# Performance work log

Measured on AMD Instinct MI355X. Metric: run time of the kernel, lower is better.

The kernel has to match this reference:

```python
import jax, jax.numpy as jnp
import numpy as np

# Module config (matches init_kwargs)
T = 4096          # max_seq_length == runtime seq len
L = 1024          # local_size
BQ = 16           # block_q (q bucket size in flash loop)
BK = 128          # block_k (k bucket size in flash loop)
C = 128           # query chunk size used for the banded jax formulation (multiple of BQ, == BK)
NC = T // C       # number of query chunks
W = L + C         # key window width per query chunk: [chunk_start - L, chunk_start + C)
HEAD_DIM = 64
NUM_HEAD = 16
SCALE = 1.0 / float(np.sqrt(HEAD_DIM))


def _build_mask():
    # Reproduces the flash path's sparsity: a (q,k) pair is kept iff
    #   j <= i  (element-level causal) AND
    #   k_block_start(j) >= q_block_start(i) - local_size  (block skip rule)
    # where q_block_start = (i//BQ)*BQ, k_block_start = (j//BK)*BK.
    i_loc = np.arange(C)                      # query offset inside chunk
    j_rel = np.arange(W) - L                  # key offset relative to chunk start
    causal = j_rel[None, :] <= i_loc[:, None]
    kb = (j_rel // BK) * BK                   # floor-div works for negatives
    qb = (i_loc // BQ) * BQ
    local_ok = kb[None, :] >= qb[:, None] - L
    static = causal & local_ok                # [C, W], chunk-independent
    starts = np.arange(NC) * C
    valid = (starts[:, None] + j_rel[None, :]) >= 0   # mask out left padding
    return jnp.asarray(static[None, :, :] & valid[:, None, :])  # [NC, C, W]

MASK = _build_mask()


def setup_inputs() -> dict:
    key = jax.random.key(0)
    k1, k2, k3 = jax.random.split(key, 3)
    B = 2
    E = NUM_HEAD * HEAD_DIM
    q = jax.random.normal(k1, (T, B, E), jnp.float32)
    k = jax.random.normal(k2, (T, B, E), jnp.float32)
    v = jax.random.normal(k3, (T, B, E), jnp.float32)
    padding_mask = jnp.zeros((B, T), bool)     # unused by module's forward
    attention_mask = jnp.zeros((B, T), bool)   # unused by module's forward
    return {"q": q, "k": k, "v": v, "padding_mask": padding_mask, "attention_mask": attention_mask}


def _attend(qh, kh, vh):
    # qh/kh/vh: [BH, T, D]; banded local+causal attention
    BH, _, D = qh.shape
    qr = (qh * SCALE).reshape(BH, NC, C, D)
    kp = jnp.pad(kh, ((0, 0), (L, 0), (0, 0)))
    vp = jnp.pad(vh, ((0, 0), (L, 0), (0, 0)))
    # window gather: chunk c covers padded indices [c*C, c*C + W)
    idx = jnp.arange(NC)[:, None] * C + jnp.arange(W)[None, :]   # [NC, W]
    kw = kp[:, idx]   # [BH, NC, W, D]
    vw = vp[:, idx]   # [BH, NC, W, D]
    s = jnp.einsum('bcid,bcjd->bcij', qr, kw)      # [BH, NC, C, W]
    s = jnp.where(MASK, s, -jnp.inf)
    p = jax.nn.softmax(s, axis=-1)                 # every row has a valid (diagonal) entry
    o = jnp.einsum('bcij,bcjd->bcid', p, vw)
    return o.reshape(BH, T, D)


def reference(q, k, v, padding_mask, attention_mask):
    Tq, B, E = q.shape
    # (T, B, H*D) -> (B*H, T, D), matching view(T, B*H, D).transpose(0,1)
    qh = q.reshape(Tq, B * NUM_HEAD, HEAD_DIM).transpose(1, 0, 2)
    kh = k.reshape(Tq, B * NUM_HEAD, HEAD_DIM).transpose(1, 0, 2)
    vh = v.reshape(Tq, B * NUM_HEAD, HEAD_DIM).transpose(1, 0, 2)
    o = _attend(qh, kh, vh)                        # [B*H, T, D]
    # out.transpose(0,1).view(T, B, H*D)
    return o.transpose(1, 0, 2).reshape(Tq, B, E)
```

## Files before the change

### kernel.cpp

```cpp
#include <hip/hip_runtime.h>
#include <hip/hip_bf16.h>

typedef float f32x16 __attribute__((ext_vector_type(16)));
typedef short bf16x8 __attribute__((ext_vector_type(8)));

#define SCALE2 0.1803368801111242f

#define EXP2(x) __builtin_amdgcn_exp2f(x)

static __device__ __forceinline__ unsigned int pk2(float a, float b) {
  unsigned short lo = __builtin_bit_cast(unsigned short, __float2bfloat16(a));
  unsigned short hi = __builtin_bit_cast(unsigned short, __float2bfloat16(b));
  return (unsigned int)lo | ((unsigned int)hi << 16);
}

#define GLDS16(g, l) __builtin_amdgcn_global_load_lds(                      \
    (const __attribute__((address_space(1))) unsigned int*)(g),             \
    (__attribute__((address_space(3))) unsigned int*)(l), 16, 0, 0)

extern "C" __global__ __launch_bounds__(256)
void prep_qk(const float* __restrict__ q, const float* __restrict__ k,
             char* __restrict__ qs, char* __restrict__ ks)
{
  int idx = blockIdx.x * 256 + threadIdx.x;
  const bool isK = idx >= (1 << 20);
  idx &= (1 << 20) - 1;
  const int fb  = idx * 8;
  const int t   = fb >> 11;
  const int rem = fb & 2047;
  const int bh  = rem >> 6;
  const int d0  = rem & 63;
  const float* sp = (isK ? k : q) + fb;
  const float4 f0 = *(const float4*)sp;
  const float4 f1 = *(const float4*)(sp + 4);
  uint4 u;
  if (isK) {
    u.x = pk2(f0.x, f0.y); u.y = pk2(f0.z, f0.w);
    u.z = pk2(f1.x, f1.y); u.w = pk2(f1.z, f1.w);
    const size_t ob = (size_t)bh * 524288 + (size_t)t * 128 + ((d0 * 2) ^ ((t & 7) << 4));
    *(uint4*)(ks + ob) = u;
  } else {
    u.x = pk2(f0.x * SCALE2, f0.y * SCALE2); u.y = pk2(f0.z * SCALE2, f0.w * SCALE2);
    u.z = pk2(f1.x * SCALE2, f1.y * SCALE2); u.w = pk2(f1.z * SCALE2, f1.w * SCALE2);
    const size_t ob = (size_t)bh * 524288 + (size_t)t * 128 + d0 * 2;
    *(uint4*)(qs + ob) = u;
  }
}

extern "C" __global__ __launch_bounds__(256)
void prep_v(const float* __restrict__ v, char* __restrict__ vts)
{
  __shared__ float Lt[64 * 65];
  const int bh   = blockIdx.x >> 6;
  const int tile = blockIdx.x & 63;
  const int t0   = tile * 64;
  const int b = bh >> 4, h = bh & 15;
  const float* vp = v + (size_t)t0 * 2048 + b * 1024 + h * 64;
  const int tid = threadIdx.x;
  const int dd = tid & 63, tl = tid >> 6;
  #pragma unroll
  for (int p2 = 0; p2 < 16; ++p2) {
    const int t_loc = p2 * 4 + tl;
    Lt[dd * 65 + t_loc] = vp[(size_t)t_loc * 2048 + dd];
  }
  __syncthreads();
  const int d = tid >> 2, tg = tid & 3;
  float a[16];
  #pragma unroll
  for (int j = 0; j < 16; ++j) a[j] = Lt[d * 65 + tg * 16 + j];
  uint4 u0, u1;
  u0.x = pk2(a[0], a[1]);  u0.y = pk2(a[2], a[3]);
  u0.z = pk2(a[4], a[5]);  u0.w = pk2(a[6], a[7]);
  u1.x = pk2(a[8], a[9]);  u1.y = pk2(a[10], a[11]);
  u1.z = pk2(a[12], a[13]); u1.w = pk2(a[14], a[15]);
  const size_t ob = (size_t)bh * 524288 + (size_t)d * 8192;
  const int off0 = t0 * 2 + tg * 32;
  const int swz = (d & 7) << 4;
  *(uint4*)(vts + ob + ((off0) ^ swz))      = u0;
  *(uint4*)(vts + ob + ((off0 + 16) ^ swz)) = u1;
}

extern "C" __global__ __launch_bounds__(256, 4)
void sparse_attn7(const char* __restrict__ qs, const char* __restrict__ ks,
                  const char* __restrict__ vts, float* __restrict__ og)
{
  __shared__ __align__(16) char lds[32768];

  const int w    = blockIdx.x;
  const int work = (w & 7) * 128 + (w >> 3);
  const int c    = work & 31;
  const int bh   = work >> 5;

  const int tid = threadIdx.x;
  const int wv  = tid >> 6;
  const int ln  = tid & 63;
  const int l31 = ln & 31;
  const int hi  = ln >> 5;

  const int ql = wv * 32 + l31;
  const int qt = c * 128 + ql;
  const size_t hb = (size_t)bh * 524288;

  bf16x8 qf[4];
  {
    const char* qp = qs + hb + (size_t)qt * 128 + hi * 16;
    #pragma unroll
    for (int kd = 0; kd < 4; ++kd)
      qf[kd] = *(const bf16x8*)(qp + kd * 32);
  }

  f32x16 ot[2];
  #pragma unroll
  for (int i = 0; i < 2; ++i)
    #pragma unroll
    for (int r = 0; r < 16; ++r) ot[i][r] = 0.f;

  float lsum = 0.f;

  const int n0 = (c >= 8) ? 0 : (16 - 2 * c);

  const char* kga = ks  + hb + (size_t)((2 * c - 16 + n0) * 64) * 128
                    + (wv * 2) * 1024 + ln * 16;
  const char* vga = vts + hb + (size_t)((wv * 2) * 8 + (ln >> 3)) * 8192
                    + (size_t)((2 * c - 16 + n0) * 64) * 2 + (ln & 7) * 16;

  auto STAGE = [&](int p) {
    char* kl = lds + p * 16384 + wv * 2048;
    char* vl = lds + p * 16384 + 8192 + wv * 2048;
    GLDS16(kga,            kl);
    GLDS16(kga + 1024,     kl + 1024);
    GLDS16(vga,            vl);
    GLDS16(vga + 8 * 8192, vl + 1024);
  };

  STAGE(0);
  kga += 8192; vga += 128;
  __syncthreads();

  int p = 0;
  for (int n = n0; n <= 17; ++n) {
    if (n < 17) {
      STAGE(p ^ 1);
      kga += 8192; vga += 128;
    }

    const bool skip = ((n <= 1) && (wv > 0)) || ((n == 17) && (wv < 2));
    if (!skip) {
      const char* Kl = lds + p * 16384;
      const char* Vt = lds + p * 16384 + 8192;

      f32x16 st[2];
      #pragma unroll
      for (int mt = 0; mt < 2; ++mt)
        #pragma unroll
        for (int r = 0; r < 16; ++r) st[mt][r] = 0.f;

      __builtin_amdgcn_s_setprio(1);
      #pragma unroll
      for (int kd = 0; kd < 4; ++kd) {
        #pragma unroll
        for (int mt = 0; mt < 2; ++mt) {
          const int key  = mt * 32 + l31;
          const int boff = (key * 128 + kd * 32 + hi * 16) ^ ((key & 7) << 4);
          const bf16x8 kf = *(const bf16x8*)(Kl + boff);
          st[mt] = __builtin_amdgcn_mfma_f32_32x32x16_bf16(kf, qf[kd], st[mt], 0, 0, 0);
        }
      }
      __builtin_amdgcn_s_setprio(0);

      if (n >= 16 && wv * 32 < (n - 16) * 64 + 64) {
        const int base = (n - 16) * 64;
        #pragma unroll
        for (int mt = 0; mt < 2; ++mt)
          #pragma unroll
          for (int r = 0; r < 16; ++r) {
            const int kl2 = base + mt * 32 + (r & 3) + 8 * (r >> 2) + 4 * hi;
            if (kl2 > ql) st[mt][r] = -1e30f;
          }
      }

      const bool dead = (n <= 1) && (l31 >= 16);
      if (!dead) {
        #pragma unroll
        for (int mt = 0; mt < 2; ++mt)
          #pragma unroll
          for (int r = 0; r < 16; ++r)
            st[mt][r] = EXP2(st[mt][r]);
      } else {
        #pragma unroll
        for (int mt = 0; mt < 2; ++mt)
          #pragma unroll
          for (int r = 0; r < 16; ++r) st[mt][r] = 0.f;
      }

      #pragma unroll
      for (int mt = 0; mt < 2; ++mt) {
        #pragma unroll
        for (int s = 0; s < 2; ++s) {
          const unsigned int X0 = pk2(st[mt][s * 8 + 0], st[mt][s * 8 + 1]);
          const unsigned int X1 = pk2(st[mt][s * 8 + 2], st[mt][s * 8 + 3]);
          const unsigned int Y0 = pk2(st[mt][s * 8 + 4], st[mt][s * 8 + 5]);
          const unsigned int Y1 = pk2(st[mt][s * 8 + 6], st[mt][s * 8 + 7]);
          const unsigned int s0 = hi ? X0 : Y0;
          const unsigned int s1 = hi ? X1 : Y1;
          const unsigned int r0 = (unsigned int)__shfl_xor((int)s0, 32);
          const unsigned int r1 = (unsigned int)__shfl_xor((int)s1, 32);
          uint4 u;
          if (hi == 0) { u.x = X0; u.y = X1; u.z = r0; u.w = r1; }
          else         { u.x = r0; u.y = r1; u.z = Y0; u.w = Y1; }
          const bf16x8 pf = __builtin_bit_cast(bf16x8, u);
          const int ks2 = mt * 2 + s;
          __builtin_amdgcn_s_setprio(1);
          #pragma unroll
          for (int dt = 0; dt < 2; ++dt) {
            const int d    = dt * 32 + l31;
            const int boff = d * 128 + ((ks2 * 32 + hi * 16) ^ ((d & 7) << 4));
            const bf16x8 vf = *(const bf16x8*)(Vt + boff);
            ot[dt] = __builtin_amdgcn_mfma_f32_32x32x16_bf16(vf, pf, ot[dt], 0, 0, 0);
          }
          __builtin_amdgcn_s_setprio(0);
        }
      }

      if (!dead) {
        float t[16];
        #pragma unroll
        for (int r = 0; r < 16; ++r) t[r] = st[0][r] + st[1][r];
        #pragma unroll
        for (int s2 = 8; s2 >= 1; s2 >>= 1)
          #pragma unroll
          for (int r = 0; r < 8; ++r)
            if (r < s2) t[r] += t[r + s2];
        lsum += t[0];
      }
    }

    __syncthreads();
    p ^= 1;
  }

  float lt = lsum + __shfl_xor(lsum, 32);
  const float rl = 1.0f / lt;

  const int hoff = ((bh >> 4) * 1024) + ((bh & 15) * 64);
  float* op = og + (size_t)qt * 2048 + hoff;
  #pragma unroll
  for (int dt = 0; dt < 2; ++dt)
    #pragma unroll
    for (int g = 0; g < 4; ++g) {
      float4 o4;
      o4.x = ot[dt][g * 4 + 0] * rl;
      o4.y = ot[dt][g * 4 + 1] * rl;
      o4.z = ot[dt][g * 4 + 2] * rl;
      o4.w = ot[dt][g * 4 + 3] * rl;
      *(float4*)(op + dt * 32 + g * 8 + hi * 4) = o4;
    }
}

extern "C" __global__ __launch_bounds__(256)
void sparse_attn_v1(const float* __restrict__ qg, const float* __restrict__ kg,
                    const float* __restrict__ vg, float* __restrict__ og)
{
  __shared__ unsigned short Kl[128 * 64];
  __shared__ unsigned short Vt[64 * 128];

  const int bx  = blockIdx.x;
  const int c   = bx & 31;
  const int bh  = bx >> 5;
  const int b   = bh >> 4;
  const int h   = bh & 15;

  const int tid = threadIdx.x;
  const int wv  = tid >> 6;
  const int ln  = tid & 63;
  const int l31 = ln & 31;
  const int hi  = ln >> 5;

  const int ql = wv * 32 + l31;
  const int qt = c * 128 + ql;
  const size_t hoff = (size_t)b * 1024 + (size_t)h * 64;

  bf16x8 qf[4];
  {
    const float* qp = qg + (size_t)qt * 2048 + hoff;
    #pragma unroll
    for (int kd = 0; kd < 4; ++kd) {
      const int d0 = kd * 16 + hi * 8;
      const float4 f0 = *(const float4*)(qp + d0);
      const float4 f1 = *(const float4*)(qp + d0 + 4);
      uint4 u;
      u.x = pk2(f0.x * SCALE2, f0.y * SCALE2);
      u.y = pk2(f0.z * SCALE2, f0.w * SCALE2);
      u.z = pk2(f1.x * SCALE2, f1.y * SCALE2);
      u.w = pk2(f1.z * SCALE2, f1.w * SCALE2);
      qf[kd] = __builtin_bit_cast(bf16x8, u);
    }
  }

  f32x16 ot[2];
  #pragma unroll
  for (int i = 0; i < 2; ++i)
    #pragma unroll
    for (int r = 0; r < 16; ++r) ot[i][r] = 0.f;

  float m_run = -1e30f, l_run = 0.f;

  const int n0 = (c >= 8) ? 0 : (8 - c);
  for (int n = n0; n <= 8; ++n) {
    const int ka = (c - 8 + n) * 128;

    __syncthreads();
    {
      const int key = tid & 127;
      const int dh  = tid >> 7;
      const float* kp = kg + (size_t)(ka + key) * 2048 + hoff + dh * 32;
      #pragma unroll
      for (int u2 = 0; u2 < 4; ++u2) {
        const float4 f0 = *(const float4*)(kp + u2 * 8);
        const float4 f1 = *(const float4*)(kp + u2 * 8 + 4);
        uint4 w2;
        w2.x = pk2(f0.x, f0.y); w2.y = pk2(f0.z, f0.w);
        w2.z = pk2(f1.x, f1.y); w2.w = pk2(f1.z, f1.w);
        const int boff = (key * 128 + dh * 64 + u2 * 16) ^ ((key & 7) << 4);
        *(uint4*)((char*)Kl + boff) = w2;
      }
    }
    {
      const int kp2 = tid & 63;
      const int dq  = tid >> 6;
      const float* vp = vg + (size_t)(ka + kp2 * 2) * 2048 + hoff + dq * 16;
      float va[16], vb[16];
      #pragma unroll
      for (int u2 = 0; u2 < 4; ++u2) {
        *(float4*)(va + u2 * 4) = *(const float4*)(vp + u2 * 4);
        *(float4*)(vb + u2 * 4) = *(const float4*)(vp + 2048 + u2 * 4);
      }
      #pragma unroll
      for (int j = 0; j < 16; ++j) {
        const int d = dq * 16 + j;
        const unsigned int wrd = pk2(va[j], vb[j]);
        const int boff = d * 256 + ((kp2 * 4) ^ ((d & 7) << 4));
        *(unsigned int*)((char*)Vt + boff) = wrd;
      }
    }
    __syncthreads();

    if (n == 0 && wv > 0) continue;

    f32x16 st[4];
    #pragma unroll
    for (int mt = 0; mt < 4; ++mt)
      #pragma unroll
      for (int r = 0; r < 16; ++r) st[mt][r] = 0.f;

    #pragma unroll
    for (int kd = 0; kd < 4; ++kd) {
      #pragma unroll
      for (int mt = 0; mt < 4; ++mt) {
        const int key  = mt * 32 + l31;
        const int boff = (key * 128 + kd * 32 + hi * 16) ^ ((key & 7) << 4);
        const bf16x8 kf = *(const bf16x8*)((const char*)Kl + boff);
        st[mt] = __builtin_amdgcn_mfma_f32_32x32x16_bf16(kf, qf[kd], st[mt], 0, 0, 0);
      }
    }

    if (n == 8) {
      #pragma unroll
      for (int mt = 0; mt < 4; ++mt)
        #pragma unroll
        for (int r = 0; r < 16; ++r) {
          const int kl = mt * 32 + (r & 3) + 8 * (r >> 2) + 4 * hi;
          if (kl > ql) st[mt][r] = -1e30f;
        }
    }

    const bool dead = (n == 0) && (l31 >= 16);
    float alpha = 1.f;
    if (!dead) {
      float pm = -1e30f;
      #pragma unroll
      for (int mt = 0; mt < 4; ++mt)
        #pragma unroll
        for (int r = 0; r < 16; ++r) pm = fmaxf(pm, st[mt][r]);
      pm = fmaxf(pm, __shfl_xor(pm, 32));
      const float m_new = fmaxf(m_run, pm);
      alpha = exp2f(m_run - m_new);
      float ps = 0.f;
      #pragma unroll
      for (int mt = 0; mt < 4; ++mt)
        #pragma unroll
        for (int r = 0; r < 16; ++r) {
          const float pv = exp2f(st[mt][r] - m_new);
          st[mt][r] = pv;
          ps += pv;
        }
      ps += __shfl_xor(ps, 32);
      l_run = l_run * alpha + ps;
      m_run = m_new;
    } else {
      #pragma unroll
      for (int mt = 0; mt < 4; ++mt)
        #pragma unroll
        for (int r = 0; r < 16; ++r) st[mt][r] = 0.f;
    }
    ot[0] *= alpha;
    ot[1] *= alpha;

    #pragma unroll
    for (int mt = 0; mt < 4; ++mt) {
      #pragma unroll
      for (int s = 0; s < 2; ++s) {
        const unsigned int X0 = pk2(st[mt][s * 8 + 0], st[mt][s * 8 + 1]);
        const unsigned int X1 = pk2(st[mt][s * 8 + 2], st[mt][s * 8 + 3]);
        const unsigned int Y0 = pk2(st[mt][s * 8 + 4], st[mt][s * 8 + 5]);
        const unsigned int Y1 = pk2(st[mt][s * 8 + 6], st[mt][s * 8 + 7]);
        const unsigned int s0 = hi ? X0 : Y0;
        const unsigned int s1 = hi ? X1 : Y1;
        const unsigned int r0 = (unsigned int)__shfl_xor((int)s0, 32);
        const unsigned int r1 = (unsigned int)__shfl_xor((int)s1, 32);
        uint4 u;
        if (hi == 0) { u.x = X0; u.y = X1; u.z = r0; u.w = r1; }
        else         { u.x = r0; u.y = r1; u.z = Y0; u.w = Y1; }
        const bf16x8 pf = __builtin_bit_cast(bf16x8, u);
        const int ks = mt * 2 + s;
        #pragma unroll
        for (int dt = 0; dt < 2; ++dt) {
          const int d    = dt * 32 + l31;
          const int boff = (d * 256 + ks * 32 + hi * 16) ^ ((d & 7) << 4);
          const bf16x8 vf = *(const bf16x8*)((const char*)Vt + boff);
          ot[dt] = __builtin_amdgcn_mfma_f32_32x32x16_bf16(vf, pf, ot[dt], 0, 0, 0);
        }
      }
    }
  }

  const float rl = 1.0f / l_run;
  float* op = og + (size_t)qt * 2048 + hoff;
  #pragma unroll
  for (int dt = 0; dt < 2; ++dt)
    #pragma unroll
    for (int g = 0; g < 4; ++g) {
      float4 o4;
      o4.x = ot[dt][g * 4 + 0] * rl;
      o4.y = ot[dt][g * 4 + 1] * rl;
      o4.z = ot[dt][g * 4 + 2] * rl;
      o4.w = ot[dt][g * 4 + 3] * rl;
      *(float4*)(op + dt * 32 + g * 8 + hi * 4) = o4;
    }
}

extern "C" void kernel_launch(void* const* d_in, const int* in_sizes, int n_in,
                              void* d_out, int out_size, void* d_ws, size_t ws_size,
                              hipStream_t stream) {
  const float* q = (const float*)d_in[0];
  const float* k = (const float*)d_in[1];
  const float* v = (const float*)d_in[2];
  float* o = (float*)d_out;

  const size_t NEED = 3ull * 16777216ull;
  if (ws_size >= NEED) {
    char* qs  = (char*)d_ws;
    char* kss = qs + 16777216;
    char* vts = kss + 16777216;
    hipLaunchKernelGGL(prep_qk, dim3(8192), dim3(256), 0, stream, q, k, qs, kss);
    hipLaunchKernelGGL(prep_v,  dim3(2048), dim3(256), 0, stream, v, vts);
    hipLaunchKernelGGL(sparse_attn7, dim3(1024), dim3(256), 0, stream,
                       (const char*)qs, (const char*)kss, (const char*)vts, o);
  } else {
    hipLaunchKernelGGL(sparse_attn_v1, dim3(1024), dim3(256), 0, stream, q, k, v, o);
  }
}
```

Baseline: 93.53 us.

## Pair query chunks per 512-thread block and fuse Q conversion into attention

```diff
diff --git a/kernel.cpp b/kernel.cpp
--- a/kernel.cpp
+++ b/kernel.cpp
@@ -19,32 +19,22 @@
     (__attribute__((address_space(3))) unsigned int*)(l), 16, 0, 0)
 
 extern "C" __global__ __launch_bounds__(256)
-void prep_qk(const float* __restrict__ q, const float* __restrict__ k,
-             char* __restrict__ qs, char* __restrict__ ks)
+void prep_k(const float* __restrict__ k, char* __restrict__ ks)
 {
-  int idx = blockIdx.x * 256 + threadIdx.x;
-  const bool isK = idx >= (1 << 20);
-  idx &= (1 << 20) - 1;
+  const int idx = blockIdx.x * 256 + threadIdx.x;
   const int fb  = idx * 8;
   const int t   = fb >> 11;
   const int rem = fb & 2047;
   const int bh  = rem >> 6;
   const int d0  = rem & 63;
-  const float* sp = (isK ? k : q) + fb;
+  const float* sp = k + fb;
   const float4 f0 = *(const float4*)sp;
   const float4 f1 = *(const float4*)(sp + 4);
   uint4 u;
-  if (isK) {
-    u.x = pk2(f0.x, f0.y); u.y = pk2(f0.z, f0.w);
-    u.z = pk2(f1.x, f1.y); u.w = pk2(f1.z, f1.w);
-    const size_t ob = (size_t)bh * 524288 + (size_t)t * 128 + ((d0 * 2) ^ ((t & 7) << 4));
-    *(uint4*)(ks + ob) = u;
-  } else {
-    u.x = pk2(f0.x * SCALE2, f0.y * SCALE2); u.y = pk2(f0.z * SCALE2, f0.w * SCALE2);
-    u.z = pk2(f1.x * SCALE2, f1.y * SCALE2); u.w = pk2(f1.z * SCALE2, f1.w * SCALE2);
-    const size_t ob = (size_t)bh * 524288 + (size_t)t * 128 + d0 * 2;
-    *(uint4*)(qs + ob) = u;
-  }
+  u.x = pk2(f0.x, f0.y); u.y = pk2(f0.z, f0.w);
+  u.z = pk2(f1.x, f1.y); u.w = pk2(f1.z, f1.w);
+  const size_t ob = (size_t)bh * 524288 + (size_t)t * 128 + ((d0 * 2) ^ ((t & 7) << 4));
+  *(uint4*)(ks + ob) = u;
 }
 
 extern "C" __global__ __launch_bounds__(256)
@@ -80,33 +70,46 @@
   *(uint4*)(vts + ob + ((off0 + 16) ^ swz)) = u1;
 }
 
-extern "C" __global__ __launch_bounds__(256, 4)
-void sparse_attn7(const char* __restrict__ qs, const char* __restrict__ ks,
+extern "C" __global__ __launch_bounds__(512, 4)
+void sparse_attn8(const float* __restrict__ qg, const char* __restrict__ ks,
                   const char* __restrict__ vts, float* __restrict__ og)
 {
   __shared__ __align__(16) char lds[32768];
 
   const int w    = blockIdx.x;
-  const int work = (w & 7) * 128 + (w >> 3);
-  const int c    = work & 31;
-  const int bh   = work >> 5;
+  const int work = (w & 7) * 64 + (w >> 3);
+  const int cp   = work & 15;
+  const int bh   = work >> 4;
 
   const int tid = threadIdx.x;
-  const int wv  = tid >> 6;
+  const int wq  = tid >> 6;
+  const int g   = wq >> 2;
+  const int wv  = wq & 3;
   const int ln  = tid & 63;
   const int l31 = ln & 31;
   const int hi  = ln >> 5;
 
+  const int c  = cp * 2 + g;
   const int ql = wv * 32 + l31;
   const int qt = c * 128 + ql;
   const size_t hb = (size_t)bh * 524288;
+  const int b = bh >> 4, h = bh & 15;
 
   bf16x8 qf[4];
   {
-    const char* qp = qs + hb + (size_t)qt * 128 + hi * 16;
-    #pragma unroll
-    for (int kd = 0; kd < 4; ++kd)
-      qf[kd] = *(const bf16x8*)(qp + kd * 32);
+    const float* qp = qg + (size_t)qt * 2048 + b * 1024 + h * 64;
+    #pragma unroll
+    for (int kd = 0; kd < 4; ++kd) {
+      const int d0 = kd * 16 + hi * 8;
+      const float4 f0 = *(const float4*)(qp + d0);
+      const float4 f1 = *(const float4*)(qp + d0 + 4);
+      uint4 u;
+      u.x = pk2(f0.x * SCALE2, f0.y * SCALE2);
+      u.y = pk2(f0.z * SCALE2, f0.w * SCALE2);
+      u.z = pk2(f1.x * SCALE2, f1.y * SCALE2);
+      u.w = pk2(f1.z * SCALE2, f1.w * SCALE2);
+      qf[kd] = __builtin_bit_cast(bf16x8, u);
+    }
   }
 
   f32x16 ot[2];
@@ -117,20 +120,17 @@
 
   float lsum = 0.f;
 
-  const int n0 = (c >= 8) ? 0 : (16 - 2 * c);
-
-  const char* kga = ks  + hb + (size_t)((2 * c - 16 + n0) * 64) * 128
-                    + (wv * 2) * 1024 + ln * 16;
-  const char* vga = vts + hb + (size_t)((wv * 2) * 8 + (ln >> 3)) * 8192
-                    + (size_t)((2 * c - 16 + n0) * 64) * 2 + (ln & 7) * 16;
+  const int nr0 = (cp >= 4) ? 0 : (16 - 4 * cp);
+
+  const char* kga = ks  + hb + (size_t)((4 * cp - 16 + nr0) * 64) * 128 + tid * 16;
+  const char* vga = vts + hb + (size_t)(tid >> 3) * 8192
+                    + (size_t)((4 * cp - 16 + nr0) * 64) * 2 + (tid & 7) * 16;
 
   auto STAGE = [&](int p) {
-    char* kl = lds + p * 16384 + wv * 2048;
-    char* vl = lds + p * 16384 + 8192 + wv * 2048;
-    GLDS16(kga,            kl);
-    GLDS16(kga + 1024,     kl + 1024);
-    GLDS16(vga,            vl);
-    GLDS16(vga + 8 * 8192, vl + 1024);
+    char* kl = lds + p * 16384 + wq * 1024;
+    char* vl = lds + p * 16384 + 8192 + wq * 1024;
+    GLDS16(kga, kl);
+    GLDS16(vga, vl);
   };
 
   STAGE(0);
@@ -138,14 +138,17 @@
   __syncthreads();
 
   int p = 0;
-  for (int n = n0; n <= 17; ++n) {
-    if (n < 17) {
+  for (int nr = nr0; nr <= 19; ++nr) {
+    if (nr < 19) {
       STAGE(p ^ 1);
       kga += 8192; vga += 128;
     }
 
-    const bool skip = ((n <= 1) && (wv > 0)) || ((n == 17) && (wv < 2));
-    if (!skip) {
+    const int n = nr - 2 * g;
+    const bool act = (n >= 0) && (n <= 17)
+                  && !((n <= 1) && (wv > 0))
+                  && !((n == 17) && (wv < 2));
+    if (act) {
       const char* Kl = lds + p * 16384;
       const char* Vt = lds + p * 16384 + 8192;
 
@@ -242,18 +245,17 @@
   float lt = lsum + __shfl_xor(lsum, 32);
   const float rl = 1.0f / lt;
 
-  const int hoff = ((bh >> 4) * 1024) + ((bh & 15) * 64);
-  float* op = og + (size_t)qt * 2048 + hoff;
+  float* op = og + (size_t)qt * 2048 + b * 1024 + h * 64;
   #pragma unroll
   for (int dt = 0; dt < 2; ++dt)
     #pragma unroll
-    for (int g = 0; g < 4; ++g) {
+    for (int g2 = 0; g2 < 4; ++g2) {
       float4 o4;
-      o4.x = ot[dt][g * 4 + 0] * rl;
-      o4.y = ot[dt][g * 4 + 1] * rl;
-      o4.z = ot[dt][g * 4 + 2] * rl;
-      o4.w = ot[dt][g * 4 + 3] * rl;
-      *(float4*)(op + dt * 32 + g * 8 + hi * 4) = o4;
+      o4.x = ot[dt][g2 * 4 + 0] * rl;
+      o4.y = ot[dt][g2 * 4 + 1] * rl;
+      o4.z = ot[dt][g2 * 4 + 2] * rl;
+      o4.w = ot[dt][g2 * 4 + 3] * rl;
+      *(float4*)(op + dt * 32 + g2 * 8 + hi * 4) = o4;
     }
 }
 
@@ -457,15 +459,14 @@
   const float* v = (const float*)d_in[2];
   float* o = (float*)d_out;
 
-  const size_t NEED = 3ull * 16777216ull;
+  const size_t NEED = 2ull * 16777216ull;
   if (ws_size >= NEED) {
-    char* qs  = (char*)d_ws;
-    char* kss = qs + 16777216;
+    char* kss = (char*)d_ws;
     char* vts = kss + 16777216;
-    hipLaunchKernelGGL(prep_qk, dim3(8192), dim3(256), 0, stream, q, k, qs, kss);
-    hipLaunchKernelGGL(prep_v,  dim3(2048), dim3(256), 0, stream, v, vts);
-    hipLaunchKernelGGL(sparse_attn7, dim3(1024), dim3(256), 0, stream,
-                       (const char*)qs, (const char*)kss, (const char*)vts, o);
+    hipLaunchKernelGGL(prep_k, dim3(4096), dim3(256), 0, stream, k, kss);
+    hipLaunchKernelGGL(prep_v, dim3(2048), dim3(256), 0, stream, v, vts);
+    hipLaunchKernelGGL(sparse_attn8, dim3(512), dim3(512), 0, stream,
+                       q, (const char*)kss, (const char*)vts, o);
   } else {
     hipLaunchKernelGGL(sparse_attn_v1, dim3(1024), dim3(256), 0, stream, q, k, v, o);
   }
```

New measurement: 97.56 us. 1.04x slower.
